# Optimization experiments

Measured on AMD Instinct MI355X. Metric: run time of the kernel, lower is better.

The kernel has to match this reference:

```python
import jax, jax.numpy as jnp
import numpy as np

HIDDEN = 1408
HEADS = 16
HEAD_DIM = 88  # HIDDEN // HEADS
NUM_PATCHES = 576  # (336 // 14) ** 2
SEQ = NUM_PATCHES + 1  # +1 CLS token position in mllama4 rope cache
ROPE_BASE = 10000.0
SCALE = HEAD_DIM ** -0.5


def _rope_cos_sin():
    # Faithful to vLLM Llama4VisionRotaryEmbedding cos/sin cache.
    idx = np.arange(NUM_PATCHES, dtype=np.int64).reshape(NUM_PATCHES, 1)
    idx = np.concatenate([idx, idx[:1]], axis=0)
    idx[-1, -1] = -2  # CLS token id -> zero rotation
    n = int(np.sqrt(NUM_PATCHES))  # patches per side = 24
    fx = idx % n
    fy = idx // n
    rd = HEAD_DIM // 2  # rotary_dim = 44
    inv = 1.0 / ROPE_BASE ** (np.arange(0, rd, 2, dtype=np.float32) / rd)  # (22,)
    # repeat_interleave(2) then cat then [::2] == concat of the two 22-d halves
    freqs = np.concatenate(
        [(fx + 1)[..., None] * inv[None, None, :], (fy + 1)[..., None] * inv[None, None, :]],
        axis=-1,
    )  # (SEQ, 1, 44)
    freqs = np.where(idx.reshape(-1, 1, 1) < 0, 0.0, freqs).astype(np.float32)
    freqs = freqs.squeeze(1)  # (SEQ, 44)
    return jnp.asarray(np.cos(freqs)), jnp.asarray(np.sin(freqs))


_COS, _SIN = _rope_cos_sin()


def _apply_rope(x, cos, sin):
    # x: [B, S, H, D]; complex rotation over adjacent pairs (is_neox_style=False)
    B, S, H, D = x.shape
    xp = x.reshape(B, S, H, D // 2, 2)
    x0, x1 = xp[..., 0], xp[..., 1]
    c = cos[None, :, None, :]  # [1, S, 1, D//2]
    s = sin[None, :, None, :]
    out = jnp.stack([x0 * c - x1 * s, x0 * s + x1 * c], axis=-1)
    return out.reshape(B, S, H, D)


def setup_inputs() -> dict:
    key = jax.random.key(0)
    k1, k2, k3, k4, k5 = jax.random.split(key, 5)
    std = HIDDEN ** -0.5
    return {
        "hidden_states": jax.random.normal(k1, (32, SEQ, HIDDEN), dtype=jnp.float32),
        "w_qkv": jax.random.normal(k2, (HIDDEN, 3 * HIDDEN), dtype=jnp.float32) * std,
        "b_qkv": jax.random.normal(k3, (3 * HIDDEN,), dtype=jnp.float32) * 0.02,
        "w_o": jax.random.normal(k4, (HIDDEN, HIDDEN), dtype=jnp.float32) * std,
        "b_o": jax.random.normal(k5, (HIDDEN,), dtype=jnp.float32) * 0.02,
    }


def reference(hidden_states, w_qkv, b_qkv, w_o, b_o):
    B, S, _ = hidden_states.shape
    qkv = hidden_states @ w_qkv + b_qkv  # [B, S, 3*HIDDEN]
    q, k, v = jnp.split(qkv, 3, axis=-1)
    q = q.reshape(B, S, HEADS, HEAD_DIM)
    k = k.reshape(B, S, HEADS, HEAD_DIM)
    v = v.reshape(B, S, HEADS, HEAD_DIM)
    q = _apply_rope(q, _COS, _SIN)
    k = _apply_rope(k, _COS, _SIN)
    scores = jnp.einsum("bqhd,bkhd->bhqk", q, k) * SCALE
    probs = jax.nn.softmax(scores, axis=-1)
    attn = jnp.einsum("bhqk,bkhd->bqhd", probs, v).reshape(B, S, HIDDEN)
    return attn @ w_o + b_o
```

## Files before the change

kernel.cpp:

```cpp
#include <hip/hip_runtime.h>
#include <math.h>

#define HEADS    16
#define HEAD_DIM 88
#define SEQ      577
#define SEQV     640
#define HIDDEN   1408
#define NQKV     4224
#define NQKV_PAD 4352
#define NOUT_PAD 1536
#define RD       44
#define SCALE_F  0.1066003581778052f
#define MPAD_ROWS 18688
#define NKT      22
#define BUF_SH   32768

typedef __attribute__((ext_vector_type(8))) short bf16x8;
typedef __attribute__((ext_vector_type(4))) float f32x4;

__device__ __forceinline__ unsigned short f2bf(float x) {
    unsigned u = __float_as_uint(x);
    unsigned r = u + 0x7fff + ((u >> 16) & 1);
    return (unsigned short)(r >> 16);
}
__device__ __forceinline__ f32x4 fzero() {
    f32x4 z; z.x = 0.f; z.y = 0.f; z.z = 0.f; z.w = 0.f; return z;
}
__device__ __forceinline__ int xcd_swz(int flat, int nwg) {
    int q = nwg >> 3, r = nwg & 7;
    int x = flat & 7, j = flat >> 3;
    return (x < r ? x * (q + 1) : r * (q + 1) + (x - r) * q) + j;
}

__global__ void rope_precompute(float* __restrict__ cosb, float* __restrict__ sinb) {
    int s = blockIdx.x;
    int j = threadIdx.x;
    if (j >= RD) return;
    float c, sn;
    if (s == SEQ - 1) {
        c = 1.f; sn = 0.f;
    } else {
        int fx = s % 24, fy = s / 24;
        int p = (j < 22) ? j : j - 22;
        float inv = powf(10000.f, -(float)p / 22.f);
        float f = (float)((j < 22 ? fx : fy) + 1) * inv;
        c = cosf(f); sn = sinf(f);
    }
    cosb[s * RD + j] = c;
    sinb[s * RD + j] = sn;
}

__global__ void conv_hs(const float* __restrict__ in, unsigned short* __restrict__ out,
                        long nreal, long ntot) {
    long i = ((long)blockIdx.x * 256 + threadIdx.x) * 4;
    if (i >= ntot) return;
    ushort4 o;
    if (i < nreal) {
        float4 v = *(const float4*)(in + i);
        o = make_ushort4(f2bf(v.x), f2bf(v.y), f2bf(v.z), f2bf(v.w));
    } else {
        o = make_ushort4(0, 0, 0, 0);
    }
    *(ushort4*)(out + i) = o;
}

__global__ void conv_wT(const float* __restrict__ in, unsigned short* __restrict__ out,
                        int R, int Creal) {
    __shared__ float t[32][33];
    int bx = blockIdx.x * 32, by = blockIdx.y * 32;
    int tx = threadIdx.x & 31, ty = threadIdx.x >> 5;
    #pragma unroll
    for (int i = 0; i < 4; ++i) {
        int col = bx + tx;
        t[ty + i * 8][tx] = (col < Creal) ? in[(size_t)(by + ty + i * 8) * Creal + col] : 0.f;
    }
    __syncthreads();
    #pragma unroll
    for (int i = 0; i < 4; ++i)
        out[(size_t)(bx + ty + i * 8) * R + by + tx] = f2bf(t[tx][ty + i * 8]);
}

__device__ __forceinline__ void stage_half(const unsigned short* __restrict__ src,
                                           int kt, unsigned short* lds, int tid) {
    #pragma unroll
    for (int q = 0; q < 2; ++q) {
        int cf = tid + 512 * q;
        int r  = cf >> 3, c = cf & 7;
        int cg = c ^ (r & 7);
        __builtin_amdgcn_global_load_lds(
            (const __attribute__((address_space(1))) void*)(src + (size_t)r * HIDDEN + kt * 64 + cg * 8),
            (__attribute__((address_space(3))) void*)(lds + cf * 8),
            16, 0, 0);
    }
}

template<int N> __device__ __forceinline__ void vwait() {
    if constexpr (N >= 0)
        asm volatile("s_waitcnt vmcnt(%0)" :: "i"(N) : "memory");
}

template<int CBUF, int IH, int JH, bool STG, int SSIDE, int SHALF, int SBUF, int WAITN>
__device__ __forceinline__ void phase8(
    const unsigned short* __restrict__ wsrc, const unsigned short* __restrict__ hsrc,
    unsigned short* smem, int skt, int tid,
    int ww, int wh, int quad, int l15, f32x4 (&acc)[8][4])
{
    bf16x8 afr[4][2], bfr[2][2];
    #pragma unroll
    for (int i2 = 0; i2 < 4; ++i2)
        #pragma unroll
        for (int kk = 0; kk < 2; ++kk) {
            int r = ww * 64 + i2 * 16 + l15;
            afr[i2][kk] = *(const bf16x8*)(smem + CBUF * BUF_SH + IH * 8192
                          + r * 64 + (((kk * 4 + quad) ^ (r & 7)) << 3));
        }
    #pragma unroll
    for (int j2 = 0; j2 < 2; ++j2)
        #pragma unroll
        for (int kk = 0; kk < 2; ++kk) {
            int r = wh * 32 + j2 * 16 + l15;
            bfr[j2][kk] = *(const bf16x8*)(smem + CBUF * BUF_SH + 16384 + JH * 8192
                          + r * 64 + (((kk * 4 + quad) ^ (r & 7)) << 3));
        }
    if constexpr (STG) {
        const unsigned short* s = (SSIDE ? hsrc : wsrc) + (size_t)SHALF * 128 * HIDDEN;
        stage_half(s, skt, smem + SBUF * BUF_SH + (SSIDE ? 16384 : 0) + SHALF * 8192, tid);
    }
    __builtin_amdgcn_sched_barrier(0);
    __builtin_amdgcn_s_barrier();
    __builtin_amdgcn_sched_barrier(0);
    __builtin_amdgcn_s_setprio(1);
    #pragma unroll
    for (int i2 = 0; i2 < 4; ++i2)
        #pragma unroll
        for (int j2 = 0; j2 < 2; ++j2)
            #pragma unroll
            for (int kk = 0; kk < 2; ++kk)
                acc[IH * 4 + i2][JH * 2 + j2] = __builtin_amdgcn_mfma_f32_16x16x32_bf16(
                    afr[i2][kk], bfr[j2][kk], acc[IH * 4 + i2][JH * 2 + j2], 0, 0, 0);
    __builtin_amdgcn_s_setprio(0);
    __builtin_amdgcn_sched_barrier(0);
    vwait<WAITN>();
    __builtin_amdgcn_s_barrier();
    __builtin_amdgcn_sched_barrier(0);
}

__device__ __forceinline__ void gemm256_8ph(
    const unsigned short* __restrict__ wsrc, const unsigned short* __restrict__ hsrc,
    unsigned short* smem, int tid, f32x4 (&acc)[8][4])
{
    const int lane = tid & 63, w8 = tid >> 6;
    const int quad = lane >> 4, l15 = lane & 15;
    const int ww = w8 >> 2, wh = w8 & 3;

    stage_half(wsrc,                0, smem,                  tid);
    stage_half(hsrc,                0, smem + 16384,          tid);
    stage_half(wsrc + 128 * HIDDEN, 0, smem + 8192,           tid);
    stage_half(hsrc + 128 * HIDDEN, 0, smem + 24576,          tid);
    stage_half(wsrc,                1, smem + BUF_SH,         tid);
    stage_half(hsrc,                1, smem + BUF_SH + 16384, tid);
    asm volatile("s_waitcnt vmcnt(4)" ::: "memory");
    __builtin_amdgcn_s_barrier();
    __builtin_amdgcn_sched_barrier(0);

    for (int it = 0; it < 10; ++it) {
        int k1 = 2 * it + 1, k2 = 2 * it + 2, k3 = 2 * it + 3;
        phase8<0,0,0, true,0,1,1,  6>(wsrc, hsrc, smem, k1, tid, ww, wh, quad, l15, acc);
        phase8<0,0,1, true,1,1,1, -1>(wsrc, hsrc, smem, k1, tid, ww, wh, quad, l15, acc);
        phase8<0,1,0, true,0,0,0, -1>(wsrc, hsrc, smem, k2, tid, ww, wh, quad, l15, acc);
        phase8<0,1,1, true,1,0,0,  8>(wsrc, hsrc, smem, k2, tid, ww, wh, quad, l15, acc);
        phase8<1,0,0, true,0,1,0,  6>(wsrc, hsrc, smem, k2, tid, ww, wh, quad, l15, acc);
        phase8<1,0,1, true,1,1,0, -1>(wsrc, hsrc, smem, k2, tid, ww, wh, quad, l15, acc);
        phase8<1,1,0, true,0,0,1, -1>(wsrc, hsrc, smem, k3, tid, ww, wh, quad, l15, acc);
        phase8<1,1,1, true,1,0,1,  8>(wsrc, hsrc, smem, k3, tid, ww, wh, quad, l15, acc);
    }
    phase8<0,0,0, true,0,1,1,  6>(wsrc, hsrc, smem, 21, tid, ww, wh, quad, l15, acc);
    phase8<0,0,1, true,1,1,1, -1>(wsrc, hsrc, smem, 21, tid, ww, wh, quad, l15, acc);
    phase8<0,1,0, false,0,0,0, -1>(wsrc, hsrc, smem, 0, tid, ww, wh, quad, l15, acc);
    phase8<0,1,1, false,0,0,0,  4>(wsrc, hsrc, smem, 0, tid, ww, wh, quad, l15, acc);
    phase8<1,0,0, false,0,0,0,  0>(wsrc, hsrc, smem, 0, tid, ww, wh, quad, l15, acc);
    phase8<1,0,1, false,0,0,0, -1>(wsrc, hsrc, smem, 0, tid, ww, wh, quad, l15, acc);
    phase8<1,1,0, false,0,0,0, -1>(wsrc, hsrc, smem, 0, tid, ww, wh, quad, l15, acc);
    phase8<1,1,1, false,0,0,0, -1>(wsrc, hsrc, smem, 0, tid, ww, wh, quad, l15, acc);
}

__global__ __launch_bounds__(512, 2) void qkv_mfma(
    const unsigned short* __restrict__ hsb, const unsigned short* __restrict__ wt,
    const float* __restrict__ bias, const float* __restrict__ cosb,
    const float* __restrict__ sinb,
    unsigned short* __restrict__ qb, unsigned short* __restrict__ kb,
    unsigned short* __restrict__ vtb,
    int Mchunk, int row_off)
{
    __shared__ unsigned short smem[2 * BUF_SH];
    int tid = threadIdx.x;
    int lane = tid & 63, w8 = tid >> 6;
    int quad = lane >> 4, l15 = lane & 15;
    int ww = w8 >> 2, wh = w8 & 3;

    int nwg  = gridDim.x * gridDim.y;
    int flat = blockIdx.y * gridDim.x + blockIdx.x;
    int wg   = xcd_swz(flat, nwg);
    int n0   = (wg % gridDim.x) * 256;
    int m0   = (wg / gridDim.x) * 256;

    f32x4 acc[8][4];
    #pragma unroll
    for (int i = 0; i < 8; ++i)
        #pragma unroll
        for (int j = 0; j < 4; ++j) acc[i][j] = fzero();

    gemm256_8ph(wt + (size_t)n0 * HIDDEN,
                hsb + (size_t)(row_off + m0) * HIDDEN, smem, tid, acc);

    #pragma unroll
    for (int j = 0; j < 4; ++j) {
        int m = m0 + (j >> 1) * 128 + wh * 32 + (j & 1) * 16 + l15;
        if (m >= Mchunk) continue;
        int bb = m / SEQ;
        int s  = m - bb * SEQ;
        const float* cr = cosb + s * RD;
        const float* sr = sinb + s * RD;
        #pragma unroll
        for (int i = 0; i < 8; ++i) {
            int ng = n0 + (i >> 2) * 128 + ww * 64 + (i & 3) * 16 + quad * 4;
            if (ng >= NQKV) continue;
            int sec = ng / HIDDEN;
            int nn  = ng - sec * HIDDEN;
            int h   = nn / HEAD_DIM;
            int d0  = nn - h * HEAD_DIM;
            int bh  = bb * HEADS + h;
            f32x4 v = acc[i][j];
            const float4 bv = *(const float4*)(bias + ng);
            v.x += bv.x; v.y += bv.y; v.z += bv.z; v.w += bv.w;
            if (sec < 2) {
                int p0 = d0 >> 1;
                float c0 = cr[p0],     s0 = sr[p0];
                float c1 = cr[p0 + 1], s1 = sr[p0 + 1];
                float x0 = v.x, x1 = v.y;
                v.x = x0 * c0 - x1 * s0; v.y = x0 * s0 + x1 * c0;
                x0 = v.z; x1 = v.w;
                v.z = x0 * c1 - x1 * s1; v.w = x0 * s1 + x1 * c1;
                if (sec == 0) { v.x *= SCALE_F; v.y *= SCALE_F; v.z *= SCALE_F; v.w *= SCALE_F; }
                unsigned short* dst = (sec == 0) ? qb : kb;
                ushort4 o = make_ushort4(f2bf(v.x), f2bf(v.y), f2bf(v.z), f2bf(v.w));
                *(ushort4*)(dst + ((size_t)bh * SEQ + s) * HEAD_DIM + d0) = o;
            } else {
                unsigned short* vb = vtb + ((size_t)bh * HEAD_DIM + d0) * SEQV + s;
                vb[0]        = f2bf(v.x);
                vb[SEQV]     = f2bf(v.y);
                vb[2 * SEQV] = f2bf(v.z);
                vb[3 * SEQV] = f2bf(v.w);
            }
        }
    }
}

__global__ __launch_bounds__(512, 2) void out_mfma(
    const unsigned short* __restrict__ ab, const unsigned short* __restrict__ wt,
    const float* __restrict__ bias, float* __restrict__ out,
    int Mchunk, int row_off)
{
    __shared__ unsigned short smem[2 * BUF_SH];
    int tid = threadIdx.x;
    int lane = tid & 63, w8 = tid >> 6;
    int quad = lane >> 4, l15 = lane & 15;
    int ww = w8 >> 2, wh = w8 & 3;

    int nwg  = gridDim.x * gridDim.y;
    int flat = blockIdx.y * gridDim.x + blockIdx.x;
    int wg   = xcd_swz(flat, nwg);
    int n0   = (wg % gridDim.x) * 256;
    int m0   = (wg / gridDim.x) * 256;

    f32x4 acc[8][4];
    #pragma unroll
    for (int i = 0; i < 8; ++i)
        #pragma unroll
        for (int j = 0; j < 4; ++j) acc[i][j] = fzero();

    gemm256_8ph(wt + (size_t)n0 * HIDDEN,
                ab + (size_t)m0 * HIDDEN, smem, tid, acc);

    #pragma unroll
    for (int j = 0; j < 4; ++j) {
        int m = m0 + (j >> 1) * 128 + wh * 32 + (j & 1) * 16 + l15;
        if (m >= Mchunk) continue;
        size_t orow = (size_t)(row_off + m) * HIDDEN;
        #pragma unroll
        for (int i = 0; i < 8; ++i) {
            int nn = n0 + (i >> 2) * 128 + ww * 64 + (i & 3) * 16 + quad * 4;
            if (nn >= HIDDEN) continue;
            f32x4 v = acc[i][j];
            const float4 bv = *(const float4*)(bias + nn);
            v.x += bv.x; v.y += bv.y; v.z += bv.z; v.w += bv.w;
            *(f32x4*)(out + orow + nn) = v;
        }
    }
}

#define KTT  64
#define PSTR 72
#define RESCALE_THR 8.0f

template<bool FULL>
__device__ __forceinline__ void attn_step(
    int k0, const unsigned short* __restrict__ kg, const unsigned short* __restrict__ vg,
    unsigned short* __restrict__ Ps, int quad, int l15,
    const bf16x8 (&qf)[2][3], f32x4 (&O)[2][6], float (&m_i)[2], float (&l_i)[2])
{
    bf16x8 kf[3][4];
    #pragma unroll
    for (int ks = 0; ks < 3; ++ks)
        #pragma unroll
        for (int nf = 0; nf < 4; ++nf) {
            bf16x8 v = *(const bf16x8*)(kg +
                (size_t)(k0 + nf * 16 + l15) * HEAD_DIM + ks * 32 + quad * 8);
            if (ks == 2 && quad == 3) v = (bf16x8)(short)0;
            kf[ks][nf] = v;
        }

    f32x4 sc[2][4];
    #pragma unroll
    for (int mf = 0; mf < 2; ++mf)
        #pragma unroll
        for (int nf = 0; nf < 4; ++nf) sc[mf][nf] = fzero();
    __builtin_amdgcn_s_setprio(1);
    #pragma unroll
    for (int ks = 0; ks < 3; ++ks)
        #pragma unroll
        for (int nf = 0; nf < 4; ++nf) {
            sc[0][nf] = __builtin_amdgcn_mfma_f32_16x16x32_bf16(kf[ks][nf], qf[0][ks], sc[0][nf], 0, 0, 0);
            sc[1][nf] = __builtin_amdgcn_mfma_f32_16x16x32_bf16(kf[ks][nf], qf[1][ks], sc[1][nf], 0, 0, 0);
        }
    __builtin_amdgcn_s_setprio(0);

    bf16x8 vf[2][6];
    auto smx = [&](int mf) {
        float t[4];
        #pragma unroll
        for (int nf = 0; nf < 4; ++nf) {
            float mv[4];
            #pragma unroll
            for (int r = 0; r < 4; ++r) {
                bool valid = FULL || (k0 + nf * 16 + quad * 4 + r < SEQ);
                mv[r] = valid ? sc[mf][nf][r] : -INFINITY;
            }
            t[nf] = fmaxf(fmaxf(mv[0], mv[1]), fmaxf(mv[2], mv[3]));
        }
        float pmax = fmaxf(fmaxf(t[0], t[1]), fmaxf(t[2], t[3]));
        pmax = fmaxf(pmax, __shfl_xor(pmax, 16));
        pmax = fmaxf(pmax, __shfl_xor(pmax, 32));
        float mold = m_i[mf];
        bool skip = __all(pmax - mold <= RESCALE_THR);
        float mnew = skip ? mold : fmaxf(mold, pmax);
        float rsum = 0.f;
        #pragma unroll
        for (int nf = 0; nf < 4; ++nf) {
            ushort4 o;
            float s0 = 0.f, s1 = 0.f;
            #pragma unroll
            for (int r = 0; r < 4; ++r) {
                bool valid = FULL || (k0 + nf * 16 + quad * 4 + r < SEQ);
                float p = valid ? __expf(sc[mf][nf][r] - mnew) : 0.f;
                if (r < 2) s0 += p; else s1 += p;
                ((unsigned short*)&o)[r] = f2bf(p);
            }
            rsum += s0 + s1;
            *(ushort4*)(Ps + (mf * 16 + l15) * PSTR + nf * 16 + quad * 4) = o;
        }
        rsum += __shfl_xor(rsum, 16);
        rsum += __shfl_xor(rsum, 32);
        if (!skip) {
            float alpha = __expf(mold - mnew);
            m_i[mf] = mnew;
            l_i[mf] = l_i[mf] * alpha + rsum;
            #pragma unroll
            for (int r = 0; r < 4; ++r) {
                float ar = __shfl(alpha, quad * 4 + r, 16);
                #pragma unroll
                for (int nf = 0; nf < 6; ++nf) O[mf][nf][r] *= ar;
            }
        } else {
            l_i[mf] += rsum;
        }
    };

    smx(0);
    #pragma unroll
    for (int ks = 0; ks < 2; ++ks)
        #pragma unroll
        for (int nf = 0; nf < 6; ++nf)
            vf[ks][nf] = *(const bf16x8*)(vg +
                (size_t)(nf * 16 + l15) * SEQV + k0 + ks * 32 + quad * 8);
    smx(1);

    __builtin_amdgcn_s_setprio(1);
    #pragma unroll
    for (int ks = 0; ks < 2; ++ks) {
        bf16x8 a0 = *(const bf16x8*)(Ps + l15 * PSTR + ks * 32 + quad * 8);
        bf16x8 a1 = *(const bf16x8*)(Ps + (16 + l15) * PSTR + ks * 32 + quad * 8);
        #pragma unroll
        for (int nf = 0; nf < 6; ++nf) {
            O[0][nf] = __builtin_amdgcn_mfma_f32_16x16x32_bf16(a0, vf[ks][nf], O[0][nf], 0, 0, 0);
            O[1][nf] = __builtin_amdgcn_mfma_f32_16x16x32_bf16(a1, vf[ks][nf], O[1][nf], 0, 0, 0);
        }
    }
    __builtin_amdgcn_s_setprio(0);
}

__global__ __launch_bounds__(64, 3) void attn_mfma(
    const unsigned short* __restrict__ qb, const unsigned short* __restrict__ kb,
    const unsigned short* __restrict__ vtb, unsigned short* __restrict__ awsb)
{
    __shared__ unsigned short Ps[32 * PSTR];

    int lane = threadIdx.x;
    int quad = lane >> 4, l15 = lane & 15;

    int nwg  = gridDim.x * gridDim.y * gridDim.z;
    int flat = (blockIdx.z * gridDim.y + blockIdx.y) * gridDim.x + blockIdx.x;
    int w    = xcd_swz(flat, nwg);
    int qblk = w % gridDim.x;
    int rem  = w / gridDim.x;
    int h    = rem % gridDim.y;
    int bb   = rem / gridDim.y;
    int q0   = qblk * 32;
    int bh   = bb * HEADS + h;
    const unsigned short* qg = qb  + (size_t)bh * SEQ * HEAD_DIM;
    const unsigned short* kg = kb  + (size_t)bh * SEQ * HEAD_DIM;
    const unsigned short* vg = vtb + (size_t)bh * HEAD_DIM * SEQV;

    bf16x8 qf[2][3];
    #pragma unroll
    for (int mf = 0; mf < 2; ++mf)
        #pragma unroll
        for (int ks = 0; ks < 3; ++ks)
            qf[mf][ks] = *(const bf16x8*)(qg +
                (size_t)(q0 + mf * 16 + l15) * HEAD_DIM + ks * 32 + quad * 8);

    f32x4 O[2][6];
    float m_i[2], l_i[2];
    #pragma unroll
    for (int mf = 0; mf < 2; ++mf) {
        #pragma unroll
        for (int nf = 0; nf < 6; ++nf) O[mf][nf] = fzero();
        m_i[mf] = -INFINITY; l_i[mf] = 0.f;
    }

    for (int k0 = 0; k0 < SEQ - KTT; k0 += KTT)
        attn_step<true>(k0, kg, vg, Ps, quad, l15, qf, O, m_i, l_i);
    attn_step<false>(576, kg, vg, Ps, quad, l15, qf, O, m_i, l_i);

    #pragma unroll
    for (int mf = 0; mf < 2; ++mf) {
        #pragma unroll
        for (int r = 0; r < 4; ++r) {
            int row = q0 + mf * 16 + quad * 4 + r;
            if (row >= SEQ) continue;
            float lb = __shfl(l_i[mf], quad * 4 + r, 16);
            float il = 1.f / lb;
            size_t base = (size_t)(bb * SEQ + row) * HIDDEN + h * HEAD_DIM;
            #pragma unroll
            for (int nf = 0; nf < 6; ++nf) {
                int d = nf * 16 + l15;
                if (d < HEAD_DIM)
                    awsb[base + d] = f2bf(O[mf][nf][r] * il);
            }
        }
    }
}

extern "C" void kernel_launch(void* const* d_in, const int* in_sizes, int n_in,
                              void* d_out, int out_size, void* d_ws, size_t ws_size,
                              hipStream_t stream) {
    const float* hs    = (const float*)d_in[0];
    const float* w_qkv = (const float*)d_in[1];
    const float* b_qkv = (const float*)d_in[2];
    const float* w_o   = (const float*)d_in[3];
    const float* b_o   = (const float*)d_in[4];
    float* out = (float*)d_out;

    char* p = (char*)d_ws;
    auto alloc = [&](size_t bytes) {
        char* r = p; p += (bytes + 255) & ~(size_t)255; return r;
    };
    float*          cosb   = (float*)alloc((size_t)SEQ * RD * 4);
    float*          sinb   = (float*)alloc((size_t)SEQ * RD * 4);
    unsigned short* wqkv_t = (unsigned short*)alloc((size_t)NQKV_PAD * HIDDEN * 2);
    unsigned short* wo_t   = (unsigned short*)alloc((size_t)NOUT_PAD * HIDDEN * 2);
    unsigned short* hs_bf  = (unsigned short*)alloc((size_t)MPAD_ROWS * HIDDEN * 2);
    size_t fixed = (size_t)(p - (char*)d_ws);

    size_t per_batch = 2ull * HEADS * SEQ * HEAD_DIM * 2
                     + (size_t)HEADS * HEAD_DIM * SEQV * 2
                     + (size_t)SEQ * HIDDEN * 2;
    size_t pads = 2ull * 128 * HEAD_DIM * 2 + 24ull * SEQV * 2 + 256ull * HIDDEN * 2 + 16 * 256;
    size_t rem = (ws_size > fixed + pads) ? ws_size - fixed - pads : 0;
    int CB = (int)(rem / per_batch);
    if (CB < 1) CB = 1;
    if (CB > 32) CB = 32;

    unsigned short* qbuf  = (unsigned short*)alloc(((size_t)CB * HEADS * SEQ + 128) * HEAD_DIM * 2);
    unsigned short* kbuf  = (unsigned short*)alloc(((size_t)CB * HEADS * SEQ + 128) * HEAD_DIM * 2);
    unsigned short* vtbuf = (unsigned short*)alloc(((size_t)CB * HEADS * HEAD_DIM + 24) * SEQV * 2);
    unsigned short* awsb  = (unsigned short*)alloc(((size_t)CB * SEQ + 256) * HIDDEN * 2);

    rope_precompute<<<dim3(SEQ), dim3(64), 0, stream>>>(cosb, sinb);

    long nreal = (long)32 * SEQ * HIDDEN;
    long ntot  = (long)MPAD_ROWS * HIDDEN;
    conv_hs<<<dim3((unsigned)((ntot / 4 + 255) / 256)), 256, 0, stream>>>(hs, hs_bf, nreal, ntot);
    conv_wT<<<dim3(NQKV_PAD / 32, HIDDEN / 32), 256, 0, stream>>>(w_qkv, wqkv_t, HIDDEN, NQKV);
    conv_wT<<<dim3(NOUT_PAD / 32, HIDDEN / 32), 256, 0, stream>>>(w_o, wo_t, HIDDEN, HIDDEN);

    for (int b_off = 0; b_off < 32; b_off += CB) {
        int nb = (32 - b_off < CB) ? (32 - b_off) : CB;
        int M = nb * SEQ;

        dim3 g1(NQKV_PAD / 256, (M + 255) / 256);
        qkv_mfma<<<g1, 512, 0, stream>>>(hs_bf, wqkv_t, b_qkv, cosb, sinb,
                                         qbuf, kbuf, vtbuf, M, b_off * SEQ);
        dim3 g2((SEQ + 31) / 32, HEADS, nb);
        attn_mfma<<<g2, 64, 0, stream>>>(qbuf, kbuf, vtbuf, awsb);
        dim3 g3(NOUT_PAD / 256, (M + 255) / 256);
        out_mfma<<<g3, 512, 0, stream>>>(awsb, wo_t, b_o, out, M, b_off * SEQ);
    }
}
```

Before: 760.4 us.

## Store K and V in MFMA fragment-ordered tiles for contiguous attention loads

The QKV GEMM epilogue now writes K and V into a pre-swizzled per-64-key tile layout that matches the MFMA operand fragments. Each lane of the attention kernel can then load its bf16x8 fragment from a contiguous lane*8 offset instead of strided row gathers. The V loads also move ahead of the first softmax, and the tail tile is masked in registers. In exchange, the GEMM epilogue does scattered 2-byte V stores and more index arithmetic, and the workspace sizing changes.

Result: faster. 707.6 us (-6.9%).

```diff
diff --git a/kernel.cpp b/kernel.cpp
--- a/kernel.cpp
+++ b/kernel.cpp
@@ -14,6 +14,8 @@
 #define MPAD_ROWS 18688
 #define NKT      22
 #define BUF_SH   32768
+#define FR_TILE  6144
+#define FR_BH    61440
 
 typedef __attribute__((ext_vector_type(8))) short bf16x8;
 typedef __attribute__((ext_vector_type(4))) float f32x4;
@@ -188,8 +190,8 @@
     const unsigned short* __restrict__ hsb, const unsigned short* __restrict__ wt,
     const float* __restrict__ bias, const float* __restrict__ cosb,
     const float* __restrict__ sinb,
-    unsigned short* __restrict__ qb, unsigned short* __restrict__ kb,
-    unsigned short* __restrict__ vtb,
+    unsigned short* __restrict__ qb, unsigned short* __restrict__ kfr,
+    unsigned short* __restrict__ vfr,
     int Mchunk, int row_off)
 {
     __shared__ unsigned short smem[2 * BUF_SH];
@@ -221,6 +223,7 @@
         int s  = m - bb * SEQ;
         const float* cr = cosb + s * RD;
         const float* sr = sinb + s * RD;
+        int kt = s >> 6, sk = s & 63;
         #pragma unroll
         for (int i = 0; i < 8; ++i) {
             int ng = n0 + (i >> 2) * 128 + ww * 64 + (i & 3) * 16 + quad * 4;
@@ -241,16 +244,24 @@
                 v.x = x0 * c0 - x1 * s0; v.y = x0 * s0 + x1 * c0;
                 x0 = v.z; x1 = v.w;
                 v.z = x0 * c1 - x1 * s1; v.w = x0 * s1 + x1 * c1;
-                if (sec == 0) { v.x *= SCALE_F; v.y *= SCALE_F; v.z *= SCALE_F; v.w *= SCALE_F; }
-                unsigned short* dst = (sec == 0) ? qb : kb;
-                ushort4 o = make_ushort4(f2bf(v.x), f2bf(v.y), f2bf(v.z), f2bf(v.w));
-                *(ushort4*)(dst + ((size_t)bh * SEQ + s) * HEAD_DIM + d0) = o;
+                if (sec == 0) {
+                    v.x *= SCALE_F; v.y *= SCALE_F; v.z *= SCALE_F; v.w *= SCALE_F;
+                    ushort4 o = make_ushort4(f2bf(v.x), f2bf(v.y), f2bf(v.z), f2bf(v.w));
+                    *(ushort4*)(qb + ((size_t)bh * SEQ + s) * HEAD_DIM + d0) = o;
+                } else {
+                    ushort4 o = make_ushort4(f2bf(v.x), f2bf(v.y), f2bf(v.z), f2bf(v.w));
+                    size_t ka = ((((size_t)bh * 10 + kt) * 3 + (d0 >> 5)) * 4 + (sk >> 4)) * 512
+                              + (size_t)(((((d0 >> 3) & 3) << 4) + (sk & 15)) << 3) + (d0 & 7);
+                    *(ushort4*)(kfr + ka) = o;
+                }
             } else {
-                unsigned short* vb = vtb + ((size_t)bh * HEAD_DIM + d0) * SEQV + s;
-                vb[0]        = f2bf(v.x);
-                vb[SEQV]     = f2bf(v.y);
-                vb[2 * SEQV] = f2bf(v.z);
-                vb[3 * SEQV] = f2bf(v.w);
+                size_t vb0 = ((((size_t)bh * 10 + kt) * 2 + (sk >> 5)) * 6) * 512
+                           + (size_t)((((sk >> 3) & 3) << 4) << 3) + (sk & 7);
+                int d;
+                d = d0;     vfr[vb0 + ((d >> 4) << 9) + ((d & 15) << 3)] = f2bf(v.x);
+                d = d0 + 1; vfr[vb0 + ((d >> 4) << 9) + ((d & 15) << 3)] = f2bf(v.y);
+                d = d0 + 2; vfr[vb0 + ((d >> 4) << 9) + ((d & 15) << 3)] = f2bf(v.z);
+                d = d0 + 3; vfr[vb0 + ((d >> 4) << 9) + ((d & 15) << 3)] = f2bf(v.w);
             }
         }
     }
@@ -306,16 +317,19 @@
 template<bool FULL>
 __device__ __forceinline__ void attn_step(
     int k0, const unsigned short* __restrict__ kg, const unsigned short* __restrict__ vg,
-    unsigned short* __restrict__ Ps, int quad, int l15,
+    unsigned short* __restrict__ Ps, int lane, int quad, int l15,
     const bf16x8 (&qf)[2][3], f32x4 (&O)[2][6], float (&m_i)[2], float (&l_i)[2])
 {
+    const int kt = k0 >> 6;
+    const unsigned short* kbase = kg + (size_t)kt * FR_TILE + lane * 8;
+    const unsigned short* vbase = vg + (size_t)kt * FR_TILE + lane * 8;
+
     bf16x8 kf[3][4];
     #pragma unroll
     for (int ks = 0; ks < 3; ++ks)
         #pragma unroll
         for (int nf = 0; nf < 4; ++nf) {
-            bf16x8 v = *(const bf16x8*)(kg +
-                (size_t)(k0 + nf * 16 + l15) * HEAD_DIM + ks * 32 + quad * 8);
+            bf16x8 v = *(const bf16x8*)(kbase + ((ks * 4 + nf) << 9));
             if (ks == 2 && quad == 3) v = (bf16x8)(short)0;
             kf[ks][nf] = v;
         }
@@ -336,6 +350,23 @@
     __builtin_amdgcn_s_setprio(0);
 
     bf16x8 vf[2][6];
+    #pragma unroll
+    for (int ks = 0; ks < 2; ++ks)
+        #pragma unroll
+        for (int nf = 0; nf < 6; ++nf) {
+            bf16x8 v = *(const bf16x8*)(vbase + ((ks * 6 + nf) << 9));
+            if constexpr (!FULL) {
+                if (ks == 0 && quad == 0) {
+                    bf16x8 z = (bf16x8)(short)0;
+                    z[0] = v[0];
+                    v = z;
+                } else {
+                    v = (bf16x8)(short)0;
+                }
+            }
+            vf[ks][nf] = v;
+        }
+
     auto smx = [&](int mf) {
         float t[4];
         #pragma unroll
@@ -387,12 +418,6 @@
     };
 
     smx(0);
-    #pragma unroll
-    for (int ks = 0; ks < 2; ++ks)
-        #pragma unroll
-        for (int nf = 0; nf < 6; ++nf)
-            vf[ks][nf] = *(const bf16x8*)(vg +
-                (size_t)(nf * 16 + l15) * SEQV + k0 + ks * 32 + quad * 8);
     smx(1);
 
     __builtin_amdgcn_s_setprio(1);
@@ -410,8 +435,8 @@
 }
 
 __global__ __launch_bounds__(64, 3) void attn_mfma(
-    const unsigned short* __restrict__ qb, const unsigned short* __restrict__ kb,
-    const unsigned short* __restrict__ vtb, unsigned short* __restrict__ awsb)
+    const unsigned short* __restrict__ qb, const unsigned short* __restrict__ kfr,
+    const unsigned short* __restrict__ vfr, unsigned short* __restrict__ awsb)
 {
     __shared__ unsigned short Ps[32 * PSTR];
 
@@ -428,8 +453,8 @@
     int q0   = qblk * 32;
     int bh   = bb * HEADS + h;
     const unsigned short* qg = qb  + (size_t)bh * SEQ * HEAD_DIM;
-    const unsigned short* kg = kb  + (size_t)bh * SEQ * HEAD_DIM;
-    const unsigned short* vg = vtb + (size_t)bh * HEAD_DIM * SEQV;
+    const unsigned short* kg = kfr + (size_t)bh * FR_BH;
+    const unsigned short* vg = vfr + (size_t)bh * FR_BH;
 
     bf16x8 qf[2][3];
     #pragma unroll
@@ -449,8 +474,8 @@
     }
 
     for (int k0 = 0; k0 < SEQ - KTT; k0 += KTT)
-        attn_step<true>(k0, kg, vg, Ps, quad, l15, qf, O, m_i, l_i);
-    attn_step<false>(576, kg, vg, Ps, quad, l15, qf, O, m_i, l_i);
+        attn_step<true>(k0, kg, vg, Ps, lane, quad, l15, qf, O, m_i, l_i);
+    attn_step<false>(576, kg, vg, Ps, lane, quad, l15, qf, O, m_i, l_i);
 
     #pragma unroll
     for (int mf = 0; mf < 2; ++mf) {
@@ -492,18 +517,18 @@
     unsigned short* hs_bf  = (unsigned short*)alloc((size_t)MPAD_ROWS * HIDDEN * 2);
     size_t fixed = (size_t)(p - (char*)d_ws);
 
-    size_t per_batch = 2ull * HEADS * SEQ * HEAD_DIM * 2
-                     + (size_t)HEADS * HEAD_DIM * SEQV * 2
+    size_t per_batch = (size_t)HEADS * SEQ * HEAD_DIM * 2
+                     + 2ull * HEADS * FR_BH * 2
                      + (size_t)SEQ * HIDDEN * 2;
-    size_t pads = 2ull * 128 * HEAD_DIM * 2 + 24ull * SEQV * 2 + 256ull * HIDDEN * 2 + 16 * 256;
+    size_t pads = 128ull * HEAD_DIM * 2 + 2ull * FR_BH * 2 + 256ull * HIDDEN * 2 + 16 * 256;
     size_t rem = (ws_size > fixed + pads) ? ws_size - fixed - pads : 0;
     int CB = (int)(rem / per_batch);
     if (CB < 1) CB = 1;
     if (CB > 32) CB = 32;
 
     unsigned short* qbuf  = (unsigned short*)alloc(((size_t)CB * HEADS * SEQ + 128) * HEAD_DIM * 2);
-    unsigned short* kbuf  = (unsigned short*)alloc(((size_t)CB * HEADS * SEQ + 128) * HEAD_DIM * 2);
-    unsigned short* vtbuf = (unsigned short*)alloc(((size_t)CB * HEADS * HEAD_DIM + 24) * SEQV * 2);
+    unsigned short* kbuf  = (unsigned short*)alloc(((size_t)CB * HEADS + 1) * FR_BH * 2);
+    unsigned short* vtbuf = (unsigned short*)alloc(((size_t)CB * HEADS + 1) * FR_BH * 2);
     unsigned short* awsb  = (unsigned short*)alloc(((size_t)CB * SEQ + 256) * HIDDEN * 2);
 
     rope_precompute<<<dim3(SEQ), dim3(64), 0, stream>>>(cosb, sinb);
```
